# Optimization experiments

Measured on AMD Instinct MI355X. Metric: run time of the kernel, lower is better.

## Reference

```python
import jax, jax.numpy as jnp
import numpy as np

H, W = 512, 512
ROWS_PER_CHUNK = 32  # H must be divisible; 16 chunks
TWO_PI = 2.0 * np.pi
ALPHA_MIN = 1.0 / 255.0  # rasterizer skip threshold
ALPHA_MAX = 0.999        # rasterizer alpha clamp


def setup_inputs() -> dict:
    key = jax.random.key(0)
    k0, k1, k2, k3 = jax.random.split(key, 4)
    N = 2048
    xyz = jax.random.uniform(k0, (N, 2), jnp.float32, -1.0, 1.0)      # NDC means
    scaling = jax.random.uniform(k1, (N, 2), jnp.float32, 2.0, 12.0)  # pixel-space stds
    rotation = jax.random.normal(k2, (N, 1), jnp.float32)             # pre-sigmoid angle
    features = jax.random.uniform(k3, (N, 3), jnp.float32)            # RGB
    opacity = jnp.ones((N, 1), jnp.float32)
    return {"xyz": xyz, "scaling": scaling, "rotation": rotation,
            "features": features, "opacity": opacity}


def reference(xyz, scaling, rotation, features, opacity):
    # --- project_gaussians_2d_scale_rot ---
    theta = jax.nn.sigmoid(rotation[:, 0]) * TWO_PI          # get_rotation
    s = jnp.abs(scaling)                                      # get_scaling
    cos, sin = jnp.cos(theta), jnp.sin(theta)
    s0, s1 = s[:, 0] ** 2, s[:, 1] ** 2
    # cov = R diag(s^2) R^T  -> [[a,b],[b,c]]
    a = cos * cos * s0 + sin * sin * s1
    b = cos * sin * (s0 - s1)
    c = sin * sin * s0 + cos * cos * s1
    inv_det = 1.0 / (a * c - b * b)
    c0, c1, c2 = c * inv_det, -b * inv_det, a * inv_det       # conic = cov^-1
    # NDC [-1,1] -> pixel centers (gsplat ndc2pix)
    xys = 0.5 * ((xyz + 1.0) * jnp.array([W, H], jnp.float32) - 1.0)  # [N,2]
    op = opacity[:, 0]

    xs = jnp.arange(W, dtype=jnp.float32)
    ys = jnp.arange(H, dtype=jnp.float32)
    dx = xs[:, None] - xys[None, :, 0]                        # [W,N]
    dx2_half_c0 = 0.5 * c0 * dx * dx                          # [W,N], reused per row block

    def render_rows(yb):
        # yb: [R] row y-coordinates
        dy = yb[:, None, None] - xys[None, None, :, 1]        # [R,1,N]
        sigma = dx2_half_c0[None] + 0.5 * c2 * dy * dy + c1 * dx[None] * dy  # [R,W,N]
        alpha = jnp.minimum(ALPHA_MAX, op * jnp.exp(-sigma))
        alpha = jnp.where(alpha < ALPHA_MIN, 0.0, alpha)
        return jnp.einsum('rwn,nc->rwc', alpha, features)     # [R,W,3]

    out = jax.lax.map(render_rows, ys.reshape(-1, ROWS_PER_CHUNK))  # [C,R,W,3]
    out = jnp.clip(out.reshape(H, W, 3), 0.0, 1.0)
    return out.transpose(2, 0, 1)[None]                       # [1,3,H,W]
```

## Files before the change

### kernel.cpp

```cpp
#include <hip/hip_runtime.h>
#include <math.h>

#define W_IMG 512
#define H_IMG 512
#define ALPHA_MIN (1.0f/255.0f)
#define ALPHA_MAX 0.999f

__global__ __launch_bounds__(256) void splat_render(
    const float* __restrict__ xyz,
    const float* __restrict__ scaling,
    const float* __restrict__ rotation,
    const float* __restrict__ features,
    const float* __restrict__ opacity,
    float* __restrict__ out, int N)
{
  __shared__ float4 sA[256];
  __shared__ float4 sB[256];
  __shared__ float  sOp[256];
  __shared__ int wave_base[4];
  __shared__ int s_total;

  const int tid = threadIdx.x;
  const int tile_x = blockIdx.x << 4;
  const int tile_y = blockIdx.y << 4;
  const int lx = tid & 15, ly = tid >> 4;
  const float px = (float)(tile_x + lx);
  const float py = (float)(tile_y + ly);
  const float tx0 = (float)tile_x, tx1 = (float)(tile_x + 15);
  const float ty0 = (float)tile_y, ty1 = (float)(tile_y + 15);

  float acc0 = 0.f, acc1 = 0.f, acc2 = 0.f;

  for (int base = 0; base < N; base += 256) {
    const int gi = base + tid;
    bool keep = false;
    float mx=0.f,my=0.f,h0=0.f,h1=0.f,h2=0.f,op=0.f,f0=0.f,f1=0.f,f2=0.f;
    if (gi < N) {
      const float rx = rotation[gi];
      const float theta = 6.28318530717958647692f / (1.0f + __expf(-rx));
      float sn, cs;
      __sincosf(theta, &sn, &cs);
      const float sxa = fabsf(scaling[2*gi+0]);
      const float sya = fabsf(scaling[2*gi+1]);
      const float s0 = sxa*sxa, s1 = sya*sya;
      const float a = cs*cs*s0 + sn*sn*s1;
      const float b = cs*sn*(s0 - s1);
      const float c = sn*sn*s0 + cs*cs*s1;
      const float inv_det = 1.0f / (a*c - b*b);
      h0 = 0.5f * c * inv_det;
      h1 = -b * inv_det;
      h2 = 0.5f * a * inv_det;
      mx = 0.5f*((xyz[2*gi+0] + 1.0f)*(float)W_IMG - 1.0f);
      my = 0.5f*((xyz[2*gi+1] + 1.0f)*(float)H_IMG - 1.0f);
      op = opacity[gi];
      f0 = features[3*gi+0]; f1 = features[3*gi+1]; f2 = features[3*gi+2];
      if (op > 0.0f) {
        const float T = __logf(255.0f * op);
        if (T > 0.0f) {
          const float r2 = 2.0f * T * fmaxf(s0, s1) * 1.0001f + 1e-2f;
          const float ddx = fmaxf(fmaxf(tx0 - mx, mx - tx1), 0.0f);
          const float ddy = fmaxf(fmaxf(ty0 - my, my - ty1), 0.0f);
          keep = (ddx*ddx + ddy*ddy) <= r2;
        }
      }
    }
    const unsigned long long m = __ballot(keep);
    const int lane = tid & 63, wid = tid >> 6;
    const int pre = __popcll(m & ((1ull << lane) - 1ull));
    if (lane == 0) wave_base[wid] = __popcll(m);
    __syncthreads();
    if (tid == 0) {
      int s = 0;
      #pragma unroll
      for (int w = 0; w < 4; ++w) { const int cw = wave_base[w]; wave_base[w] = s; s += cw; }
      s_total = s;
    }
    __syncthreads();
    if (keep) {
      const int p = wave_base[wid] + pre;
      sA[p] = make_float4(mx, my, h0, h1);
      sB[p] = make_float4(h2, f0, f1, f2);
      sOp[p] = op;
    }
    __syncthreads();
    const int cnt = s_total;
    for (int j = 0; j < cnt; ++j) {
      const float4 gA = sA[j];
      const float4 gB = sB[j];
      const float opj = sOp[j];
      const float dx = px - gA.x;
      const float dy = py - gA.y;
      const float sig = fmaf(dx, fmaf(gA.z, dx, gA.w*dy), gB.x*dy*dy);
      const float e = __expf(-sig);
      float alpha = fminf(ALPHA_MAX, opj * e);
      alpha = (alpha < ALPHA_MIN) ? 0.0f : alpha;
      acc0 = fmaf(alpha, gB.y, acc0);
      acc1 = fmaf(alpha, gB.z, acc1);
      acc2 = fmaf(alpha, gB.w, acc2);
    }
    __syncthreads();
  }

  const int x = tile_x + lx, y = tile_y + ly;
  const int pix = y * W_IMG + x;
  out[pix]                 = fminf(fmaxf(acc0, 0.0f), 1.0f);
  out[W_IMG*H_IMG + pix]   = fminf(fmaxf(acc1, 0.0f), 1.0f);
  out[2*W_IMG*H_IMG + pix] = fminf(fmaxf(acc2, 0.0f), 1.0f);
}

extern "C" void kernel_launch(void* const* d_in, const int* in_sizes, int n_in,
                              void* d_out, int out_size, void* d_ws, size_t ws_size,
                              hipStream_t stream) {
  const float* xyz      = (const float*)d_in[0];
  const float* scaling  = (const float*)d_in[1];
  const float* rotation = (const float*)d_in[2];
  const float* features = (const float*)d_in[3];
  const float* opacity  = (const float*)d_in[4];
  float* out = (float*)d_out;
  const int N = in_sizes[0] / 2;
  dim3 grid(W_IMG / 16, H_IMG / 16);
  splat_render<<<grid, 256, 0, stream>>>(xyz, scaling, rotation, features, opacity, out, N);
}
```

Measured before the change: 76.20 us.

## Precompute per-Gaussian parameters in a separate kernel and drop redundant prefix sync

Moves the per-Gaussian projection (sigmoid, sincos, conic inversion, culling radius) out of the render kernel into a precompute kernel that writes packed float4 records to workspace. Each of the 1024 render tiles then loads those records instead of recomputing the transcendentals. The wave prefix offsets are now computed redundantly by every thread, which removes one __syncthreads per chunk. In exchange it adds a second kernel launch and global reads of 48 bytes per Gaussian per tile. The workspace offsets are hardcoded for N=2048, so a larger N would make the three buffers overlap.

```diff
diff --git a/kernel.cpp b/kernel.cpp
--- a/kernel.cpp
+++ b/kernel.cpp
@@ -5,20 +5,56 @@
 #define H_IMG 512
 #define ALPHA_MIN (1.0f/255.0f)
 #define ALPHA_MAX 0.999f
+#define NMAX_CHUNK 256
 
-__global__ __launch_bounds__(256) void splat_render(
+__global__ __launch_bounds__(256) void precompute_params(
     const float* __restrict__ xyz,
     const float* __restrict__ scaling,
     const float* __restrict__ rotation,
     const float* __restrict__ features,
     const float* __restrict__ opacity,
+    float4* __restrict__ G0, float4* __restrict__ G1, float4* __restrict__ G2,
+    int N)
+{
+  const int i = blockIdx.x * 256 + threadIdx.x;
+  if (i >= N) return;
+  const float rx = rotation[i];
+  const float theta = 6.28318530717958647692f / (1.0f + __expf(-rx));
+  float sn, cs;
+  __sincosf(theta, &sn, &cs);
+  const float sxa = fabsf(scaling[2*i+0]);
+  const float sya = fabsf(scaling[2*i+1]);
+  const float s0 = sxa*sxa, s1 = sya*sya;
+  const float a = cs*cs*s0 + sn*sn*s1;
+  const float b = cs*sn*(s0 - s1);
+  const float c = sn*sn*s0 + cs*cs*s1;
+  const float inv_det = 1.0f / (a*c - b*b);
+  const float h0 = 0.5f * c * inv_det;
+  const float h1 = -b * inv_det;
+  const float h2 = 0.5f * a * inv_det;
+  const float mx = 0.5f*((xyz[2*i+0] + 1.0f)*(float)W_IMG - 1.0f);
+  const float my = 0.5f*((xyz[2*i+1] + 1.0f)*(float)H_IMG - 1.0f);
+  const float op = opacity[i];
+  float r2 = -1.0f;
+  if (op > 0.0f) {
+    const float T = __logf(255.0f * op);
+    if (T > 0.0f) r2 = 2.0f * T * fmaxf(s0, s1) * 1.0001f + 1e-2f;
+  }
+  G0[i] = make_float4(mx, my, h0, h1);
+  G1[i] = make_float4(h2, r2, op, 0.0f);
+  G2[i] = make_float4(features[3*i+0], features[3*i+1], features[3*i+2], 0.0f);
+}
+
+__global__ __launch_bounds__(256) void splat_render(
+    const float4* __restrict__ G0,
+    const float4* __restrict__ G1,
+    const float4* __restrict__ G2,
     float* __restrict__ out, int N)
 {
-  __shared__ float4 sA[256];
-  __shared__ float4 sB[256];
-  __shared__ float  sOp[256];
-  __shared__ int wave_base[4];
-  __shared__ int s_total;
+  __shared__ float4 sA[NMAX_CHUNK];
+  __shared__ float4 sB[NMAX_CHUNK];
+  __shared__ float  sOp[NMAX_CHUNK];
+  __shared__ int wcnt[4];
 
   const int tid = threadIdx.x;
   const int tile_x = blockIdx.x << 4;
@@ -31,60 +67,32 @@
 
   float acc0 = 0.f, acc1 = 0.f, acc2 = 0.f;
 
-  for (int base = 0; base < N; base += 256) {
+  for (int base = 0; base < N; base += NMAX_CHUNK) {
     const int gi = base + tid;
     bool keep = false;
-    float mx=0.f,my=0.f,h0=0.f,h1=0.f,h2=0.f,op=0.f,f0=0.f,f1=0.f,f2=0.f;
+    float4 g0 = make_float4(0,0,0,0), g1 = make_float4(0,0,0,0), g2 = make_float4(0,0,0,0);
     if (gi < N) {
-      const float rx = rotation[gi];
-      const float theta = 6.28318530717958647692f / (1.0f + __expf(-rx));
-      float sn, cs;
-      __sincosf(theta, &sn, &cs);
-      const float sxa = fabsf(scaling[2*gi+0]);
-      const float sya = fabsf(scaling[2*gi+1]);
-      const float s0 = sxa*sxa, s1 = sya*sya;
-      const float a = cs*cs*s0 + sn*sn*s1;
-      const float b = cs*sn*(s0 - s1);
-      const float c = sn*sn*s0 + cs*cs*s1;
-      const float inv_det = 1.0f / (a*c - b*b);
-      h0 = 0.5f * c * inv_det;
-      h1 = -b * inv_det;
-      h2 = 0.5f * a * inv_det;
-      mx = 0.5f*((xyz[2*gi+0] + 1.0f)*(float)W_IMG - 1.0f);
-      my = 0.5f*((xyz[2*gi+1] + 1.0f)*(float)H_IMG - 1.0f);
-      op = opacity[gi];
-      f0 = features[3*gi+0]; f1 = features[3*gi+1]; f2 = features[3*gi+2];
-      if (op > 0.0f) {
-        const float T = __logf(255.0f * op);
-        if (T > 0.0f) {
-          const float r2 = 2.0f * T * fmaxf(s0, s1) * 1.0001f + 1e-2f;
-          const float ddx = fmaxf(fmaxf(tx0 - mx, mx - tx1), 0.0f);
-          const float ddy = fmaxf(fmaxf(ty0 - my, my - ty1), 0.0f);
-          keep = (ddx*ddx + ddy*ddy) <= r2;
-        }
-      }
+      g0 = G0[gi]; g1 = G1[gi]; g2 = G2[gi];
+      const float ddx = fmaxf(fmaxf(tx0 - g0.x, g0.x - tx1), 0.0f);
+      const float ddy = fmaxf(fmaxf(ty0 - g0.y, g0.y - ty1), 0.0f);
+      keep = (ddx*ddx + ddy*ddy) <= g1.y;
     }
     const unsigned long long m = __ballot(keep);
     const int lane = tid & 63, wid = tid >> 6;
     const int pre = __popcll(m & ((1ull << lane) - 1ull));
-    if (lane == 0) wave_base[wid] = __popcll(m);
+    if (lane == 0) wcnt[wid] = __popcll(m);
     __syncthreads();
-    if (tid == 0) {
-      int s = 0;
-      #pragma unroll
-      for (int w = 0; w < 4; ++w) { const int cw = wave_base[w]; wave_base[w] = s; s += cw; }
-      s_total = s;
+    int wbase = 0, total = 0;
+    #pragma unroll
+    for (int w = 0; w < 4; ++w) { const int cw = wcnt[w]; if (w < wid) wbase += cw; total += cw; }
+    if (keep) {
+      const int p = wbase + pre;
+      sA[p] = make_float4(g0.x, g0.y, g0.z, g0.w);
+      sB[p] = make_float4(g1.x, g2.x, g2.y, g2.z);
+      sOp[p] = g1.z;
     }
     __syncthreads();
-    if (keep) {
-      const int p = wave_base[wid] + pre;
-      sA[p] = make_float4(mx, my, h0, h1);
-      sB[p] = make_float4(h2, f0, f1, f2);
-      sOp[p] = op;
-    }
-    __syncthreads();
-    const int cnt = s_total;
-    for (int j = 0; j < cnt; ++j) {
+    for (int j = 0; j < total; ++j) {
       const float4 gA = sA[j];
       const float4 gB = sB[j];
       const float opj = sOp[j];
@@ -118,6 +126,14 @@
   const float* opacity  = (const float*)d_in[4];
   float* out = (float*)d_out;
   const int N = in_sizes[0] / 2;
+
+  char* ws = (char*)d_ws;
+  float4* G0 = (float4*)(ws);
+  float4* G1 = (float4*)(ws + 16*2048);
+  float4* G2 = (float4*)(ws + 32*2048);
+
+  precompute_params<<<(N + 255)/256, 256, 0, stream>>>(
+      xyz, scaling, rotation, features, opacity, G0, G1, G2, N);
   dim3 grid(W_IMG / 16, H_IMG / 16);
-  splat_render<<<grid, 256, 0, stream>>>(xyz, scaling, rotation, features, opacity, out, N);
+  splat_render<<<grid, 256, 0, stream>>>(G0, G1, G2, out, N);
 }
```

After: 73.88 us. 3.0% less time.
